# Performance work log

Measured on AMD Instinct MI355X. Metric: run time of the kernel, lower is better.

## Reference

```python
import jax, jax.numpy as jnp
import numpy as np

TEMPERATURE = 0.5
B, D = 4096, 256


def setup_inputs() -> dict:
    key = jax.random.key(0)
    k1, k2 = jax.random.split(key)
    z_i = jax.random.normal(k1, (B, D), dtype=jnp.float32)
    z_j = jax.random.normal(k2, (B, D), dtype=jnp.float32)
    return {"z_i": z_i, "z_j": z_j}


def reference(z_i, z_j):
    batch = z_i.shape[0]
    n = 2 * batch
    z = jnp.concatenate([z_i, z_j], axis=0)                      # [2B, D]
    z = z / jnp.linalg.norm(z, axis=1, keepdims=True)            # L2-normalize rows
    # cosine_similarity of unit vectors == dot product -> single GEMM
    sim = jnp.einsum('id,jd->ij', z, z) / TEMPERATURE            # [2B, 2B]
    mask = jnp.eye(n, dtype=bool)
    sim = jnp.where(mask, -jnp.inf, sim)                         # mask self-similarity
    positives = jnp.concatenate(
        [jnp.diagonal(sim, offset=batch), jnp.diagonal(sim, offset=-batch)], axis=0
    )                                                            # [2B]
    loss = -positives + jax.nn.logsumexp(sim, axis=1)            # [2B]
    return loss.mean()
```

## Files before the change

kernel.cpp:

```cpp
#include <hip/hip_runtime.h>
#include <hip/hip_bf16.h>
#include <stdint.h>
#include <stddef.h>


#define B_ROWS 4096
#define D_DIM  256
#define N_ROWS 8192
#define BM 64

typedef __bf16 bf16;
typedef bf16  bf16x8  __attribute__((ext_vector_type(8)));
typedef bf16  bf16x4  __attribute__((ext_vector_type(4)));
typedef float floatx4 __attribute__((ext_vector_type(4)));

__global__ __launch_bounds__(256) void normalize_kernel(
    const float* __restrict__ z_i, const float* __restrict__ z_j,
    bf16* __restrict__ zn, float* __restrict__ sumexp) {
  const int wave = threadIdx.x >> 6;
  const int lane = threadIdx.x & 63;
  const int row  = blockIdx.x * 4 + wave;
  const float* src = (row < B_ROWS) ? (z_i + (size_t)row * D_DIM)
                                    : (z_j + (size_t)(row - B_ROWS) * D_DIM);
  float4 v = ((const float4*)src)[lane];
  float ss = v.x * v.x + v.y * v.y + v.z * v.z + v.w * v.w;
  #pragma unroll
  for (int m = 1; m < 64; m <<= 1) ss += __shfl_xor(ss, m);
  const float rn = rsqrtf(ss);
  bf16x4 o;
  o[0] = (bf16)(v.x * rn);
  o[1] = (bf16)(v.y * rn);
  o[2] = (bf16)(v.z * rn);
  o[3] = (bf16)(v.w * rn);
  ((bf16x4*)(zn + (size_t)row * D_DIM))[lane] = o;
  if (lane == 0) sumexp[row] = 0.f;
}

__global__ __launch_bounds__(256, 4) void simexp_kernel(
    const bf16* __restrict__ zn, float* __restrict__ sumexp,
    float* __restrict__ pos) {
  __shared__ __align__(16) bf16 As[BM * D_DIM];

  const int tid   = threadIdx.x;
  const int wave  = tid >> 6;
  const int lane  = tid & 63;
  const int lcol  = lane & 15;
  const int lquad = lane >> 4;
  const int ri = blockIdx.x >> 3;
  const int cj = blockIdx.x & 7;
  const int row_base = ri * BM;
  const bool tail_block = (cj == 7 && ri < 64);
  const int niter = tail_block ? 5 : 4;

  {
    const bf16* asrc = zn + (size_t)row_base * D_DIM;
    #pragma unroll
    for (int it = 0; it < 8; ++it) {
      const int s   = it * 256 + tid;
      const int n   = s >> 5;
      const int kcs = s & 31;
      const int kc  = (kcs & 24) | ((kcs & 7) ^ (n & 7));
      __builtin_amdgcn_global_load_lds(
          (const __attribute__((address_space(1))) unsigned int*)
              (asrc + (size_t)n * D_DIM + kc * 8),
          (__attribute__((address_space(3))) unsigned int*)&As[s * 8],
          16, 0, 0);
    }
  }

  float rowsum[4][4];
  #pragma unroll
  for (int ti = 0; ti < 4; ++ti)
    #pragma unroll
    for (int r = 0; r < 4; ++r) rowsum[ti][r] = 0.f;

  const int slice_col = (wave & 1) * 32;
  const int boff0 = (slice_col + lcol) * D_DIM + lquad * 8;
  const int boff1 = (slice_col + 16 + lcol) * D_DIM + lquad * 8;

  __syncthreads();

  #pragma unroll 1
  for (int q = 0; q < niter; ++q) {
    const bool tail = (q == 4);
    if (tail && wave >= 2) break;
    const int ct = tail ? (ri + 64)
                        : ((ri + 8 * cj + 2 * q + (wave >> 1)) & 127);
    const bf16* bbase = zn + (size_t)ct * BM * D_DIM;

    floatx4 acc[4][2];
    #pragma unroll
    for (int ti = 0; ti < 4; ++ti)
      #pragma unroll
      for (int tj = 0; tj < 2; ++tj) acc[ti][tj] = floatx4{0.f, 0.f, 0.f, 0.f};

    #pragma unroll
    for (int kq = 0; kq < 8; ++kq) {
      const int kc   = kq * 4 + lquad;
      const int slot = (kc & 24) | ((kc & 7) ^ (lcol & 7));
      const bf16x8 b0 = *(const bf16x8*)(bbase + boff0 + kq * 32);
      const bf16x8 b1 = *(const bf16x8*)(bbase + boff1 + kq * 32);
      #pragma unroll
      for (int ti = 0; ti < 4; ++ti) {
        const bf16x8 a =
            *(const bf16x8*)&As[(ti * 16 + lcol) * D_DIM + slot * 8];
        acc[ti][0] = __builtin_amdgcn_mfma_f32_16x16x32_bf16(a, b0, acc[ti][0],
                                                             0, 0, 0);
        acc[ti][1] = __builtin_amdgcn_mfma_f32_16x16x32_bf16(a, b1, acc[ti][1],
                                                             0, 0, 0);
      }
    }

    const bool diagw = (cj == 0 && q == 0 && wave < 2);
    const int col_base = ct * BM + slice_col;
    float colsum[2] = {0.f, 0.f};
    #pragma unroll
    for (int ti = 0; ti < 4; ++ti) {
      #pragma unroll
      for (int tj = 0; tj < 2; ++tj) {
        #pragma unroll
        for (int r = 0; r < 4; ++r) {
          const float v = acc[ti][tj][r];
          float e = __builtin_amdgcn_exp2f(v * 2.8853900817779268f);
          if (diagw || tail) {
            const int rg = row_base + ti * 16 + lquad * 4 + r;
            const int cg = col_base + tj * 16 + lcol;
            if (diagw && cg == rg) e = 0.f;
            if (tail && cg == rg + B_ROWS) {
              pos[rg] = 2.0f * v;
              pos[cg] = 2.0f * v;
            }
          }
          rowsum[ti][r] += e;
          colsum[tj]    += e;
        }
      }
    }

    if (!diagw) {
      #pragma unroll
      for (int tj = 0; tj < 2; ++tj) {
        float cs = colsum[tj];
        cs += __shfl_xor(cs, 16);
        cs += __shfl_xor(cs, 32);
        if (lquad == 0)
          atomicAdd(&sumexp[col_base + tj * 16 + lcol], cs);
      }
    }
  }

  #pragma unroll
  for (int ti = 0; ti < 4; ++ti) {
    #pragma unroll
    for (int r = 0; r < 4; ++r) {
      float s2 = rowsum[ti][r];
      s2 += __shfl_xor(s2, 1);
      s2 += __shfl_xor(s2, 2);
      s2 += __shfl_xor(s2, 4);
      s2 += __shfl_xor(s2, 8);
      if (lcol == 0) {
        const int grow = row_base + ti * 16 + lquad * 4 + r;
        atomicAdd(&sumexp[grow], s2);
      }
    }
  }
}

__global__ __launch_bounds__(1024) void reduce_kernel(
    const float* __restrict__ sumexp, const float* __restrict__ pos,
    float* __restrict__ out) {
  __shared__ float ws[16];
  const int tid = threadIdx.x;
  float s = 0.f;
  const float ln2 = 0.6931471805599453f;
  for (int k = tid; k < N_ROWS; k += 1024)
    s += __builtin_amdgcn_logf(sumexp[k]) * ln2 - pos[k];
  #pragma unroll
  for (int m = 1; m < 64; m <<= 1) s += __shfl_xor(s, m);
  const int wave = tid >> 6, lane = tid & 63;
  if (lane == 0) ws[wave] = s;
  __syncthreads();
  if (wave == 0) {
    float t = (lane < 16) ? ws[lane] : 0.f;
    #pragma unroll
    for (int m = 1; m < 16; m <<= 1) t += __shfl_xor(t, m);
    if (lane == 0) out[0] = t * (1.0f / N_ROWS);
  }
}

extern "C" void kernel_launch(void* const* d_in, const int* in_sizes, int n_in,
                              void* d_out, int out_size, void* d_ws,
                              size_t ws_size, hipStream_t stream) {
  const float* z_i = (const float*)d_in[0];
  const float* z_j = (const float*)d_in[1];
  float* out = (float*)d_out;

  bf16* zn = (bf16*)d_ws;
  float* sumexp = (float*)((char*)d_ws + (size_t)N_ROWS * D_DIM * sizeof(bf16));
  float* pos = sumexp + N_ROWS;

  normalize_kernel<<<N_ROWS / 4, 256, 0, stream>>>(z_i, z_j, zn, sumexp);
  simexp_kernel<<<1024, 256, 0, stream>>>(zn, sumexp, pos);
  reduce_kernel<<<1, 1024, 0, stream>>>(sumexp, pos, out);
}
```

Measured before the change: 107.1 us.

## Software-pipeline B-tile global loads into registers across column tiles

Result: slower. 109.8 us (+2.5%).

```diff
diff --git a/kernel.cpp b/kernel.cpp
--- a/kernel.cpp
+++ b/kernel.cpp
@@ -36,7 +36,7 @@
   if (lane == 0) sumexp[row] = 0.f;
 }
 
-__global__ __launch_bounds__(256, 4) void simexp_kernel(
+__global__ __launch_bounds__(256, 3) void simexp_kernel(
     const bf16* __restrict__ zn, float* __restrict__ sumexp,
     float* __restrict__ pos) {
   __shared__ __align__(16) bf16 As[BM * D_DIM];
@@ -68,6 +68,10 @@
     }
   }
 
+  auto ctof = [&](int q) {
+    return (q == 4) ? (ri + 64) : ((ri + 8 * cj + 2 * q + (wave >> 1)) & 127);
+  };
+
   float rowsum[4][4];
   #pragma unroll
   for (int ti = 0; ti < 4; ++ti)
@@ -77,6 +81,16 @@
   const int slice_col = (wave & 1) * 32;
   const int boff0 = (slice_col + lcol) * D_DIM + lquad * 8;
   const int boff1 = (slice_col + 16 + lcol) * D_DIM + lquad * 8;
+
+  bf16x8 bp[8];
+  {
+    const bf16* bb = zn + (size_t)ctof(0) * BM * D_DIM;
+    #pragma unroll
+    for (int k = 0; k < 4; ++k) {
+      bp[2 * k]     = *(const bf16x8*)(bb + boff0 + k * 32);
+      bp[2 * k + 1] = *(const bf16x8*)(bb + boff1 + k * 32);
+    }
+  }
 
   __syncthreads();
 
@@ -84,8 +98,7 @@
   for (int q = 0; q < niter; ++q) {
     const bool tail = (q == 4);
     if (tail && wave >= 2) break;
-    const int ct = tail ? (ri + 64)
-                        : ((ri + 8 * cj + 2 * q + (wave >> 1)) & 127);
+    const int ct = ctof(q);
     const bf16* bbase = zn + (size_t)ct * BM * D_DIM;
 
     floatx4 acc[4][2];
@@ -94,20 +107,51 @@
       #pragma unroll
       for (int tj = 0; tj < 2; ++tj) acc[ti][tj] = floatx4{0.f, 0.f, 0.f, 0.f};
 
-    #pragma unroll
-    for (int kq = 0; kq < 8; ++kq) {
+    bf16x8 bc[8];
+    #pragma unroll
+    for (int i = 0; i < 8; ++i) bc[i] = bp[i];
+    #pragma unroll
+    for (int k = 0; k < 4; ++k) {
+      bp[2 * k]     = *(const bf16x8*)(bbase + boff0 + (k + 4) * 32);
+      bp[2 * k + 1] = *(const bf16x8*)(bbase + boff1 + (k + 4) * 32);
+    }
+    #pragma unroll
+    for (int kq = 0; kq < 4; ++kq) {
       const int kc   = kq * 4 + lquad;
       const int slot = (kc & 24) | ((kc & 7) ^ (lcol & 7));
-      const bf16x8 b0 = *(const bf16x8*)(bbase + boff0 + kq * 32);
-      const bf16x8 b1 = *(const bf16x8*)(bbase + boff1 + kq * 32);
       #pragma unroll
       for (int ti = 0; ti < 4; ++ti) {
         const bf16x8 a =
             *(const bf16x8*)&As[(ti * 16 + lcol) * D_DIM + slot * 8];
-        acc[ti][0] = __builtin_amdgcn_mfma_f32_16x16x32_bf16(a, b0, acc[ti][0],
-                                                             0, 0, 0);
-        acc[ti][1] = __builtin_amdgcn_mfma_f32_16x16x32_bf16(a, b1, acc[ti][1],
-                                                             0, 0, 0);
+        acc[ti][0] = __builtin_amdgcn_mfma_f32_16x16x32_bf16(
+            a, bc[2 * kq], acc[ti][0], 0, 0, 0);
+        acc[ti][1] = __builtin_amdgcn_mfma_f32_16x16x32_bf16(
+            a, bc[2 * kq + 1], acc[ti][1], 0, 0, 0);
+      }
+    }
+
+    #pragma unroll
+    for (int i = 0; i < 8; ++i) bc[i] = bp[i];
+    if (q + 1 < niter) {
+      const bf16* bb2 = zn + (size_t)ctof(q + 1) * BM * D_DIM;
+      #pragma unroll
+      for (int k = 0; k < 4; ++k) {
+        bp[2 * k]     = *(const bf16x8*)(bb2 + boff0 + k * 32);
+        bp[2 * k + 1] = *(const bf16x8*)(bb2 + boff1 + k * 32);
+      }
+    }
+    #pragma unroll
+    for (int kq = 4; kq < 8; ++kq) {
+      const int kc   = kq * 4 + lquad;
+      const int slot = (kc & 24) | ((kc & 7) ^ (lcol & 7));
+      #pragma unroll
+      for (int ti = 0; ti < 4; ++ti) {
+        const bf16x8 a =
+            *(const bf16x8*)&As[(ti * 16 + lcol) * D_DIM + slot * 8];
+        acc[ti][0] = __builtin_amdgcn_mfma_f32_16x16x32_bf16(
+            a, bc[2 * (kq - 4)], acc[ti][0], 0, 0, 0);
+        acc[ti][1] = __builtin_amdgcn_mfma_f32_16x16x32_bf16(
+            a, bc[2 * (kq - 4) + 1], acc[ti][1], 0, 0, 0);
       }
     }
 
```

## Prefetch B tiles into registers with double-buffered inline-asm loads

Applied to the files above, without the earlier changes.

New measurement: 108.7 us. No clear change (+1.5%).

```diff
diff --git a/kernel.cpp b/kernel.cpp
--- a/kernel.cpp
+++ b/kernel.cpp
@@ -13,6 +13,15 @@
 typedef bf16  bf16x8  __attribute__((ext_vector_type(8)));
 typedef bf16  bf16x4  __attribute__((ext_vector_type(4)));
 typedef float floatx4 __attribute__((ext_vector_type(4)));
+typedef int   intx4   __attribute__((ext_vector_type(4)));
+
+#define GLOADO(dst, p, o) \
+  asm volatile("global_load_dwordx4 %0, %1, off offset:" o \
+               : "=v"(dst) : "v"(p))
+#define WAIT8(g) \
+  asm volatile("s_waitcnt vmcnt(8)" \
+               : "+v"(g[0]), "+v"(g[1]), "+v"(g[2]), "+v"(g[3]), \
+                 "+v"(g[4]), "+v"(g[5]), "+v"(g[6]), "+v"(g[7]))
 
 __global__ __launch_bounds__(256) void normalize_kernel(
     const float* __restrict__ z_i, const float* __restrict__ z_j,
@@ -36,10 +45,11 @@
   if (lane == 0) sumexp[row] = 0.f;
 }
 
-__global__ __launch_bounds__(256, 4) void simexp_kernel(
+__global__ __launch_bounds__(256, 3) void simexp_kernel(
     const bf16* __restrict__ zn, float* __restrict__ sumexp,
     float* __restrict__ pos) {
   __shared__ __align__(16) bf16 As[BM * D_DIM];
+  __shared__ float cbuf[4][5][2][16];
 
   const int tid   = threadIdx.x;
   const int wave  = tid >> 6;
@@ -50,7 +60,7 @@
   const int cj = blockIdx.x & 7;
   const int row_base = ri * BM;
   const bool tail_block = (cj == 7 && ri < 64);
-  const int niter = tail_block ? 5 : 4;
+  const int my_niter = (tail_block && wave < 2) ? 5 : 4;
 
   {
     const bf16* asrc = zn + (size_t)row_base * D_DIM;
@@ -78,15 +88,29 @@
   const int boff0 = (slice_col + lcol) * D_DIM + lquad * 8;
   const int boff1 = (slice_col + 16 + lcol) * D_DIM + lquad * 8;
 
+  intx4 g0[8], g1[8];
+  {
+    const int ct0 = (ri + 8 * cj + (wave >> 1)) & 127;
+    const bf16* bb = zn + (size_t)ct0 * BM * D_DIM;
+    const bf16* p0 = bb + boff0;
+    const bf16* p1 = bb + boff1;
+    GLOADO(g0[0], p0, "0");   GLOADO(g0[1], p1, "0");
+    GLOADO(g0[2], p0, "64");  GLOADO(g0[3], p1, "64");
+    GLOADO(g0[4], p0, "128"); GLOADO(g0[5], p1, "128");
+    GLOADO(g0[6], p0, "192"); GLOADO(g0[7], p1, "192");
+    GLOADO(g1[0], p0, "256"); GLOADO(g1[1], p1, "256");
+    GLOADO(g1[2], p0, "320"); GLOADO(g1[3], p1, "320");
+    GLOADO(g1[4], p0, "384"); GLOADO(g1[5], p1, "384");
+    GLOADO(g1[6], p0, "448"); GLOADO(g1[7], p1, "448");
+  }
+
   __syncthreads();
 
   #pragma unroll 1
-  for (int q = 0; q < niter; ++q) {
+  for (int q = 0; q < my_niter; ++q) {
     const bool tail = (q == 4);
-    if (tail && wave >= 2) break;
     const int ct = tail ? (ri + 64)
                         : ((ri + 8 * cj + 2 * q + (wave >> 1)) & 127);
-    const bf16* bbase = zn + (size_t)ct * BM * D_DIM;
 
     floatx4 acc[4][2];
     #pragma unroll
@@ -94,22 +118,55 @@
       #pragma unroll
       for (int tj = 0; tj < 2; ++tj) acc[ti][tj] = floatx4{0.f, 0.f, 0.f, 0.f};
 
-    #pragma unroll
-    for (int kq = 0; kq < 8; ++kq) {
+    const int nq  = (q + 1 < my_niter) ? q + 1 : q;
+    const int nct = (nq == 4) ? (ri + 64)
+                              : ((ri + 8 * cj + 2 * nq + (wave >> 1)) & 127);
+    const bf16* nb  = zn + (size_t)nct * BM * D_DIM;
+    const bf16* np0 = nb + boff0;
+    const bf16* np1 = nb + boff1;
+
+    WAIT8(g0);
+    #pragma unroll
+    for (int kq = 0; kq < 4; ++kq) {
       const int kc   = kq * 4 + lquad;
       const int slot = (kc & 24) | ((kc & 7) ^ (lcol & 7));
-      const bf16x8 b0 = *(const bf16x8*)(bbase + boff0 + kq * 32);
-      const bf16x8 b1 = *(const bf16x8*)(bbase + boff1 + kq * 32);
       #pragma unroll
       for (int ti = 0; ti < 4; ++ti) {
         const bf16x8 a =
             *(const bf16x8*)&As[(ti * 16 + lcol) * D_DIM + slot * 8];
-        acc[ti][0] = __builtin_amdgcn_mfma_f32_16x16x32_bf16(a, b0, acc[ti][0],
-                                                             0, 0, 0);
-        acc[ti][1] = __builtin_amdgcn_mfma_f32_16x16x32_bf16(a, b1, acc[ti][1],
-                                                             0, 0, 0);
-      }
-    }
+        acc[ti][0] = __builtin_amdgcn_mfma_f32_16x16x32_bf16(
+            a, __builtin_bit_cast(bf16x8, g0[2 * kq]), acc[ti][0], 0, 0, 0);
+        acc[ti][1] = __builtin_amdgcn_mfma_f32_16x16x32_bf16(
+            a, __builtin_bit_cast(bf16x8, g0[2 * kq + 1]), acc[ti][1],
+            0, 0, 0);
+      }
+    }
+    GLOADO(g0[0], np0, "0");   GLOADO(g0[1], np1, "0");
+    GLOADO(g0[2], np0, "64");  GLOADO(g0[3], np1, "64");
+    GLOADO(g0[4], np0, "128"); GLOADO(g0[5], np1, "128");
+    GLOADO(g0[6], np0, "192"); GLOADO(g0[7], np1, "192");
+
+    WAIT8(g1);
+    #pragma unroll
+    for (int kq = 4; kq < 8; ++kq) {
+      const int kc   = kq * 4 + lquad;
+      const int slot = (kc & 24) | ((kc & 7) ^ (lcol & 7));
+      #pragma unroll
+      for (int ti = 0; ti < 4; ++ti) {
+        const bf16x8 a =
+            *(const bf16x8*)&As[(ti * 16 + lcol) * D_DIM + slot * 8];
+        acc[ti][0] = __builtin_amdgcn_mfma_f32_16x16x32_bf16(
+            a, __builtin_bit_cast(bf16x8, g1[2 * (kq - 4)]), acc[ti][0],
+            0, 0, 0);
+        acc[ti][1] = __builtin_amdgcn_mfma_f32_16x16x32_bf16(
+            a, __builtin_bit_cast(bf16x8, g1[2 * (kq - 4) + 1]), acc[ti][1],
+            0, 0, 0);
+      }
+    }
+    GLOADO(g1[0], np0, "256"); GLOADO(g1[1], np1, "256");
+    GLOADO(g1[2], np0, "320"); GLOADO(g1[3], np1, "320");
+    GLOADO(g1[4], np0, "384"); GLOADO(g1[5], np1, "384");
+    GLOADO(g1[6], np0, "448"); GLOADO(g1[7], np1, "448");
 
     const bool diagw = (cj == 0 && q == 0 && wave < 2);
     const int col_base = ct * BM + slice_col;
@@ -136,16 +193,34 @@
         }
       }
     }
-
-    if (!diagw) {
-      #pragma unroll
-      for (int tj = 0; tj < 2; ++tj) {
-        float cs = colsum[tj];
-        cs += __shfl_xor(cs, 16);
-        cs += __shfl_xor(cs, 32);
-        if (lquad == 0)
-          atomicAdd(&sumexp[col_base + tj * 16 + lcol], cs);
-      }
+    float cs0 = colsum[0];
+    cs0 += __shfl_xor(cs0, 16);
+    cs0 += __shfl_xor(cs0, 32);
+    float cs1 = colsum[1];
+    cs1 += __shfl_xor(cs1, 16);
+    cs1 += __shfl_xor(cs1, 32);
+    if (lane < 16) {
+      cbuf[wave][q][0][lane] = cs0;
+      cbuf[wave][q][1][lane] = cs1;
+    }
+  }
+
+  asm volatile("s_waitcnt vmcnt(0)" ::: "memory");
+  __syncthreads();
+
+  {
+    const int totq = tail_block ? 5 : 4;
+    for (int idx = tid; idx < totq * 128; idx += 256) {
+      const int lc = idx & 15;
+      const int tj = (idx >> 4) & 1;
+      const int w  = (idx >> 5) & 3;
+      const int q  = idx >> 7;
+      if (q == 4 && w >= 2) continue;
+      if (q == 0 && cj == 0 && w < 2) continue;
+      const int ct = (q == 4) ? (ri + 64)
+                              : ((ri + 8 * cj + 2 * q + (w >> 1)) & 127);
+      const int col = ct * BM + (w & 1) * 32 + tj * 16 + lc;
+      atomicAdd(&sumexp[col], cbuf[w][q][tj][lc]);
     }
   }
 
```
